# Kernel tuning notes

Measured on AMD Instinct MI355X. Metric: run time of the kernel, lower is better.

Reference implementation:

```python
import jax, jax.numpy as jnp
import numpy as np

B, S, DIM, HEADS, DH = 1, 192, 512, 8, 64
LN_EPS = 1e-5


def setup_inputs() -> dict:
    key = jax.random.key(0)
    ks = jax.random.split(key, 5)
    rn = lambda k, shp: jax.random.normal(k, shp, dtype=jnp.float32) * 0.02
    return {
        "x": jax.random.normal(ks[0], (B, S, DIM), dtype=jnp.float32),
        "ln_w": jnp.ones((DIM,), jnp.float32),
        "ln_b": jnp.zeros((DIM,), jnp.float32),
        "W_abcde": rn(ks[1], (5 * HEADS * DH, DIM)),
        "b_abcde": jnp.zeros((5 * HEADS * DH,), jnp.float32),
        "W_K": rn(ks[2], (HEADS, DH, DH, DH)),
        "W_V": rn(ks[3], (HEADS, DH, DH, DH)),
        "W_out": rn(ks[4], (DIM, HEADS * DH)),
        "b_out": jnp.zeros((DIM,), jnp.float32),
    }


def reference(x, ln_w, ln_b, W_abcde, b_abcde, W_K, W_V, W_out, b_out):
    b, n, _ = x.shape
    # LayerNorm (biased variance, eps=1e-5, affine)
    mu = jnp.mean(x, axis=-1, keepdims=True)
    var = jnp.var(x, axis=-1, keepdims=True)
    xn = (x - mu) / jnp.sqrt(var + LN_EPS) * ln_w + ln_b
    # abcde projection, chunk into 5, split heads -> [b, n, h, d]
    proj = xn @ W_abcde.T + b_abcde
    a_, b_, c_, d_, e_ = [t.reshape(b, n, HEADS, DH) for t in jnp.split(proj, 5, axis=-1)]
    # cubic attention score chain (note: heads summed out in step2, reintroduced by a_)
    step1 = jnp.einsum('brnk,nijk->brij', c_, W_K)          # [b, r, d, d]
    step2 = jnp.einsum('brij,bqnj->briq', step1, b_)        # [b, r, d, q] (sum over heads of b_)
    attn = jnp.einsum('briq,bpni->bnpqr', step2, a_)        # [b, h, p, q, r]
    # "causal" mask: positions where p >= q set to 1e-6 (faithful to masked_fill_)
    t_idx = jnp.arange(n)[:, None, None]
    s_idx = jnp.arange(n)[None, :, None]
    mask = (t_idx >= s_idx)[None, None]                      # [1,1,p,q,1]
    attn = jnp.where(mask, jnp.float32(1e-6), attn)
    # 'b n p1 p2 p3 -> b n p3 (p1 p2)', scale by 1/dim_head, softmax over (p1 p2)
    attn = attn.transpose(0, 1, 4, 2, 3).reshape(b, HEADS, n, n * n) / DH
    attn = jax.nn.softmax(attn, axis=-1)
    # pairwise values: [b, p1, p2, h, d] -> 'b p s n h -> b n h (p s)'
    v = jnp.einsum('bpnh,bqng,nhgf->bpqnf', d_, e_, W_V)
    v = v.transpose(0, 3, 4, 1, 2).reshape(b, HEADS, DH, n * n)
    # weighted sum over pair axis, merge heads
    z = jnp.einsum('bnql,bnhl->bqnh', attn, v).reshape(b, n, HEADS * DH)
    return z @ W_out.T + b_out
```

## Files before the change

kernel.cpp:

```cpp
#include <hip/hip_runtime.h>
#include <hip/hip_bf16.h>
#include <cstdint>

#define SEQ 192

typedef float f32x4 __attribute__((ext_vector_type(4)));
typedef float f32x8 __attribute__((ext_vector_type(8)));
typedef __bf16 bf16;
typedef __bf16 bf16x8 __attribute__((ext_vector_type(8)));
typedef __bf16 bf16x4 __attribute__((ext_vector_type(4)));

#define MFMA_BF16(a, b, c) __builtin_amdgcn_mfma_f32_16x16x32_bf16(a, b, c, 0, 0, 0)

__device__ __forceinline__ bf16x8 cvt8(f32x8 v) {
  bf16x8 o;
#pragma unroll
  for (int i = 0; i < 8; i++) o[i] = (bf16)v[i];
  return o;
}

__global__ __launch_bounds__(256) void k1_prep(
    const float* __restrict__ x, const float* __restrict__ ln_w, const float* __restrict__ ln_b,
    const float* __restrict__ WV, bf16* __restrict__ xn_bf, bf16* __restrict__ WVt2) {
  int bid = blockIdx.x, tid = threadIdx.x;
  if (bid < 512) {
    int g = bid & 63, hh = bid >> 6;
    __shared__ float ld[64 * 65];
    int f = tid & 63, r4 = tid >> 6;
#pragma unroll
    for (int it = 0; it < 16; it++) {
      int hp = it * 4 + r4;
      ld[hp * 65 + f] = WV[(((size_t)(hh * 64 + hp) * 64 + g) * 64) + f];
    }
    __syncthreads();
    int hp2 = tid & 63;
#pragma unroll
    for (int it = 0; it < 16; it++) {
      int ff = it * 4 + r4;
      WVt2[(size_t)hh * 262144 + (size_t)(ff * 64 + g) * 64 + hp2] = (bf16)ld[hp2 * 65 + ff];
    }
    return;
  }
  bid -= 512;
  {
    int r = bid;
    const float* xr = x + (size_t)r * 512;
    float v0 = xr[tid], v1 = xr[tid + 256];
    float s = v0 + v1, s2 = v0 * v0 + v1 * v1;
#pragma unroll
    for (int off = 32; off > 0; off >>= 1) {
      s += __shfl_down(s, off);
      s2 += __shfl_down(s2, off);
    }
    __shared__ float redS[4], redS2[4];
    int wave = tid >> 6, lane = tid & 63;
    if (lane == 0) { redS[wave] = s; redS2[wave] = s2; }
    __syncthreads();
    float S = redS[0] + redS[1] + redS[2] + redS[3];
    float S2 = redS2[0] + redS2[1] + redS2[2] + redS2[3];
    float mean = S * (1.0f / 512.0f);
    float var = S2 * (1.0f / 512.0f) - mean * mean;
    float rstd = rsqrtf(var + 1e-5f);
    bf16* xnr = xn_bf + (size_t)r * 512;
    xnr[tid] = (bf16)((v0 - mean) * rstd * ln_w[tid] + ln_b[tid]);
    xnr[tid + 256] = (bf16)((v1 - mean) * rstd * ln_w[tid + 256] + ln_b[tid + 256]);
  }
}

template <int MODE>
__device__ __forceinline__ void gemm_body(const bf16* __restrict__ A, const bf16* __restrict__ Bt,
                                          bf16* __restrict__ C1, int N, int K,
                                          int nb, int mb, int tid) {
  int n0 = nb * 64, m0 = mb * 64;
  int wave = tid >> 6, lane = tid & 63;
  int lq = lane >> 4, l16 = lane & 15;
  const bf16* Ap = A + (size_t)(m0 + wave * 16 + l16) * K;
  f32x4 acc[4];
#pragma unroll
  for (int nt = 0; nt < 4; nt++) acc[nt] = (f32x4){0.f, 0.f, 0.f, 0.f};
  for (int k0 = 0; k0 < K; k0 += 32) {
    bf16x8 af = *(const bf16x8*)(Ap + k0 + lq * 8);
#pragma unroll
    for (int nt = 0; nt < 4; nt++) {
      bf16x8 bv = *(const bf16x8*)(Bt + (size_t)(n0 + nt * 16 + l16) * K + k0 + lq * 8);
      acc[nt] = MFMA_BF16(af, bv, acc[nt]);
    }
  }
  int cm = m0 + wave * 16 + lq * 4;
#pragma unroll
  for (int nt = 0; nt < 4; nt++) {
    int n = n0 + nt * 16 + l16;
    if constexpr (MODE == 1) {
#pragma unroll
      for (int rg = 0; rg < 4; rg++) C1[(size_t)(cm + rg) * N + n] = (bf16)acc[nt][rg];
    } else {
      int r = cm >> 6, i0 = cm & 63;
      bf16x4 pk = {(bf16)acc[nt][0], (bf16)acc[nt][1], (bf16)acc[nt][2], (bf16)acc[nt][3]};
      *(bf16x4*)(C1 + (size_t)r * 12288 + (size_t)n * 64 + i0) = pk;
    }
  }
}

__global__ __launch_bounds__(256) void k2_proj(
    const bf16* __restrict__ xn_bf, const float* __restrict__ Wab,
    const float* __restrict__ b_abcde, float* __restrict__ proj, bf16* __restrict__ a_bf,
    bf16* __restrict__ c_bf, bf16* __restrict__ d_bf) {
  int bid = blockIdx.x, tid = threadIdx.x;
  int nb = bid % 40, mb = bid / 40;
  int n0 = nb * 64, m0 = mb * 64;
  int wave = tid >> 6, lane = tid & 63;
  int lq = lane >> 4, l16 = lane & 15;
  const bf16* Ap = xn_bf + (size_t)(m0 + wave * 16 + l16) * 512;
  f32x4 acc[4];
#pragma unroll
  for (int nt = 0; nt < 4; nt++) acc[nt] = (f32x4){0.f, 0.f, 0.f, 0.f};
  for (int k0 = 0; k0 < 512; k0 += 32) {
    bf16x8 af = *(const bf16x8*)(Ap + k0 + lq * 8);
#pragma unroll
    for (int nt = 0; nt < 4; nt++) {
      f32x8 wv = *(const f32x8*)(Wab + (size_t)(n0 + nt * 16 + l16) * 512 + k0 + lq * 8);
      acc[nt] = MFMA_BF16(af, cvt8(wv), acc[nt]);
    }
  }
  int cm = m0 + wave * 16 + lq * 4;
#pragma unroll
  for (int nt = 0; nt < 4; nt++) {
    int n = n0 + nt * 16 + l16;
    int chunk = n >> 9, hcol = (n >> 6) & 7, i = n & 63;
#pragma unroll
    for (int rg = 0; rg < 4; rg++) {
      int m = cm + rg;
      float v = acc[nt][rg] + b_abcde[n];
      proj[(size_t)m * 2560 + n] = v;
      bf16 bv = (bf16)v;
      if (chunk == 0) a_bf[((size_t)hcol * SEQ + m) * 64 + i] = bv;
      else if (chunk == 2) c_bf[(size_t)m * 512 + (n - 1024)] = bv;
      else if (chunk == 3) d_bf[((size_t)hcol * SEQ + m) * 64 + i] = bv;
    }
  }
}

__global__ __launch_bounds__(256) void k3_mid(
    const bf16* __restrict__ c_bf, const float* __restrict__ WK, bf16* __restrict__ s1bf,
    const bf16* __restrict__ d_bf, const bf16* __restrict__ WVt2, bf16* __restrict__ tTt,
    const float* __restrict__ proj, bf16* __restrict__ eT_bf, float* __restrict__ ecum,
    bf16* __restrict__ bsum_bf) {
  __shared__ float el[64 * 65];
  int bid = blockIdx.x, tid = threadIdx.x;
  if (bid < 192) {
    int nb = bid % 64, mb = bid / 64;
    int n0 = nb * 64, m0 = mb * 64;
    int wave = tid >> 6, lane = tid & 63;
    int lq = lane >> 4, l16 = lane & 15;
    const bf16* Ap = c_bf + (size_t)(m0 + wave * 16 + l16) * 512;
    f32x4 acc[4];
#pragma unroll
    for (int nt = 0; nt < 4; nt++) acc[nt] = (f32x4){0.f, 0.f, 0.f, 0.f};
    size_t offn[4];
#pragma unroll
    for (int nt = 0; nt < 4; nt++) {
      int n = n0 + nt * 16 + l16;
      offn[nt] = (size_t)(n >> 6) * 4096 + (size_t)(n & 63) * 64;
    }
    for (int k0 = 0; k0 < 512; k0 += 32) {
      bf16x8 af = *(const bf16x8*)(Ap + k0 + lq * 8);
      size_t kb = (size_t)(k0 >> 6) * 262144 + (k0 & 32) + lq * 8;
#pragma unroll
      for (int nt = 0; nt < 4; nt++) {
        f32x8 wv = *(const f32x8*)(WK + kb + offn[nt]);
        acc[nt] = MFMA_BF16(af, cvt8(wv), acc[nt]);
      }
    }
    int cm = m0 + wave * 16 + lq * 4;
#pragma unroll
    for (int nt = 0; nt < 4; nt++) {
      int n = n0 + nt * 16 + l16;
#pragma unroll
      for (int rg = 0; rg < 4; rg++) s1bf[(size_t)(cm + rg) * 4096 + n] = (bf16)acc[nt][rg];
    }
    return;
  }
  bid -= 192;
  if (bid < 1536) {
    int h = bid / 192, rem = bid % 192;
    gemm_body<1>(d_bf + (size_t)h * 12288, WVt2 + (size_t)h * 262144,
                 tTt + (size_t)h * 786432, 4096, 64, rem % 64, rem / 64, tid);
    return;
  }
  bid -= 1536;
  if (bid < 8) {
    int h = bid;
    float carry = 0.f;
    for (int ch = 0; ch < 3; ch++) {
      int pbase = ch * 64;
      for (int idx = tid; idx < 4096; idx += 256) {
        int pl = idx >> 6, g = idx & 63;
        el[pl * 65 + g] = proj[(size_t)(pbase + pl) * 2560 + 2048 + h * 64 + g];
      }
      __syncthreads();
      for (int idx = tid; idx < 4096; idx += 256) {
        int g = idx >> 6, ql = idx & 63;
        eT_bf[((size_t)h * 64 + g) * SEQ + pbase + ql] = (bf16)el[ql * 65 + g];
      }
      if (tid < 64) {
        float run = carry;
        for (int pl = 0; pl < 64; pl++) {
          run += el[pl * 65 + tid];
          ecum[(size_t)h * 12288 + (pbase + pl) * 64 + tid] = run;
        }
        carry = run;
      }
      __syncthreads();
    }
    return;
  }
  bid -= 8;
  {
    int j = tid & 63, qg = tid >> 6;
#pragma unroll
    for (int qi = 0; qi < 16; qi++) {
      int q = bid * 64 + qg * 16 + qi;
      float s = 0.f;
#pragma unroll
      for (int hh = 0; hh < 8; hh++) s += proj[(size_t)q * 2560 + 512 + hh * 64 + j];
      bsum_bf[q * 64 + j] = (bf16)s;
    }
  }
}

__global__ __launch_bounds__(256) void k4_step2(const bf16* __restrict__ s1bf,
                                                const bf16* __restrict__ bsum_bf,
                                                bf16* __restrict__ s2bf) {
  int bid = blockIdx.x;
  gemm_body<2>(s1bf, bsum_bf, s2bf, 192, 64, bid % 3, bid / 3, threadIdx.x);
}

__global__ __launch_bounds__(256, 3) void k5_attn(
    const bf16* __restrict__ a_bf, const bf16* __restrict__ s2bf,
    const bf16* __restrict__ eT_bf, const float* __restrict__ ecum,
    bf16* __restrict__ ew_bf, float* __restrict__ Lsum) {
  int r = blockIdx.x, h = blockIdx.y;
  int tid = threadIdx.x, wave = tid >> 6, lane = tid & 63;
  int lq = lane >> 4, l16 = lane & 15;
  __shared__ __align__(16) bf16 wch[2][4][3][16 * 40];
  __shared__ float redL[4];
  int pt[3] = {wave, wave + 4, 11 - wave};

  const bf16* ah = a_bf + (size_t)h * 12288;
  const bf16* s2r = s2bf + (size_t)r * 12288;
  const bf16* eh = eT_bf + (size_t)h * 12288;
  const float* ech = ecum + (size_t)h * 12288;

  bf16x8 afr[3][2];
#pragma unroll
  for (int mt = 0; mt < 3; mt++)
#pragma unroll
    for (int kc = 0; kc < 2; kc++)
      afr[mt][kc] = *(const bf16x8*)(ah + (pt[mt] * 16 + l16) * 64 + kc * 32 + lq * 8);

  f32x4 ewacc[3][4];
#pragma unroll
  for (int mt = 0; mt < 3; mt++)
#pragma unroll
    for (int nt = 0; nt < 4; nt++) ewacc[mt][nt] = (f32x4){0.f, 0.f, 0.f, 0.f};
  float lpart = 0.f;

  for (int c = 0; c < 6; c++) {
    if (c * 32 + 31 <= wave * 16) continue;
    int par = c & 1;
    bf16x8 efr[4];
#pragma unroll
    for (int nt = 0; nt < 4; nt++)
      efr[nt] = *(const bf16x8*)(eh + (nt * 16 + l16) * SEQ + c * 32 + lq * 8);
    bf16x8 bq[2][2];
#pragma unroll
    for (int sub = 0; sub < 2; sub++) {
      int q = c * 32 + sub * 16 + l16;
      bq[sub][0] = *(const bf16x8*)(s2r + q * 64 + lq * 8);
      bq[sub][1] = *(const bf16x8*)(s2r + q * 64 + 32 + lq * 8);
    }
    f32x4 sacc[3][2];
#pragma unroll
    for (int mt = 0; mt < 3; mt++) {
      if (c * 32 + 31 <= pt[mt] * 16) continue;
#pragma unroll
      for (int sub = 0; sub < 2; sub++) {
        if (c * 32 + sub * 16 + 15 <= pt[mt] * 16) continue;
        f32x4 sv = (f32x4){0.f, 0.f, 0.f, 0.f};
        sv = MFMA_BF16(afr[mt][0], bq[sub][0], sv);
        sacc[mt][sub] = MFMA_BF16(afr[mt][1], bq[sub][1], sv);
      }
    }
#pragma unroll
    for (int mt = 0; mt < 3; mt++) {
      if (c * 32 + 31 <= pt[mt] * 16) continue;
      bf16* mybuf = &wch[par][wave][mt][0];
#pragma unroll
      for (int sub = 0; sub < 2; sub++) {
        if (c * 32 + sub * 16 + 15 <= pt[mt] * 16) {
#pragma unroll
          for (int rg = 0; rg < 4; rg++) mybuf[(lq * 4 + rg) * 40 + sub * 16 + l16] = (bf16)0.f;
          continue;
        }
        int q = c * 32 + sub * 16 + l16;
        int p0 = pt[mt] * 16 + lq * 4;
#pragma unroll
        for (int rg = 0; rg < 4; rg++) {
          float wv = (q > p0 + rg) ? __expf(sacc[mt][sub][rg] * 0.015625f) : 0.f;
          lpart += wv;
          mybuf[(lq * 4 + rg) * 40 + sub * 16 + l16] = (bf16)wv;
        }
      }
    }
#pragma unroll
    for (int mt = 0; mt < 3; mt++) {
      if (c * 32 + 31 <= pt[mt] * 16) continue;
      bf16x8 wf = *(const bf16x8*)(&wch[par][wave][mt][l16 * 40 + lq * 8]);
#pragma unroll
      for (int nt = 0; nt < 4; nt++) ewacc[mt][nt] = MFMA_BF16(wf, efr[nt], ewacc[mt][nt]);
    }
  }

  bf16* ewout = ew_bf + ((size_t)h * SEQ + r) * 12288;
#pragma unroll
  for (int mt = 0; mt < 3; mt++)
#pragma unroll
    for (int nt = 0; nt < 4; nt++)
#pragma unroll
      for (int rg = 0; rg < 4; rg++) {
        int p = pt[mt] * 16 + lq * 4 + rg;
        int g = nt * 16 + l16;
        ewout[p * 64 + g] = (bf16)(ewacc[mt][nt][rg] + ech[p * 64 + g]);
      }

#pragma unroll
  for (int off = 32; off > 0; off >>= 1) lpart += __shfl_down(lpart, off);
  if (lane == 0) redL[wave] = lpart;
  __syncthreads();
  if (tid == 0) Lsum[h * SEQ + r] = redL[0] + redL[1] + redL[2] + redL[3];
}

__global__ __launch_bounds__(512) void k5b_z(
    const bf16* __restrict__ ew_bf, const bf16* __restrict__ tTt, float* __restrict__ Zpart) {
  int h = blockIdx.x, mt = blockIdx.y, ks = blockIdx.z;
  int tid = threadIdx.x, wave = tid >> 6, lane = tid & 63;
  int lq = lane >> 4, l16 = lane & 15;
  __shared__ float zred[8][16][66];
  const bf16* ewh = ew_bf + ((size_t)h * SEQ + mt * 32) * 12288;
  const bf16* th = tTt + (size_t)h * 786432;
  f32x4 acc[2][4];
#pragma unroll
  for (int m2 = 0; m2 < 2; m2++)
#pragma unroll
    for (int nt = 0; nt < 4; nt++) acc[m2][nt] = (f32x4){0.f, 0.f, 0.f, 0.f};
  for (int jj = 0; jj < 6; jj++) {
    int kc = ks * 48 + wave * 6 + jj;
    int p = kc >> 1, g0 = (kc & 1) * 32;
    bf16x8 af0 = *(const bf16x8*)(ewh + (size_t)l16 * 12288 + kc * 32 + lq * 8);
    bf16x8 af1 = *(const bf16x8*)(ewh + (size_t)(16 + l16) * 12288 + kc * 32 + lq * 8);
#pragma unroll
    for (int nt = 0; nt < 4; nt++) {
      bf16x8 tf = *(const bf16x8*)(th + (size_t)p * 4096 + (nt * 16 + l16) * 64 + g0 + lq * 8);
      acc[0][nt] = MFMA_BF16(af0, tf, acc[0][nt]);
      acc[1][nt] = MFMA_BF16(af1, tf, acc[1][nt]);
    }
  }
#pragma unroll
  for (int m2 = 0; m2 < 2; m2++) {
    if (m2) __syncthreads();
#pragma unroll
    for (int nt = 0; nt < 4; nt++)
#pragma unroll
      for (int rg = 0; rg < 4; rg++) zred[wave][lq * 4 + rg][nt * 16 + l16] = acc[m2][nt][rg];
    __syncthreads();
#pragma unroll
    for (int o = 0; o < 2; o++) {
      int idx = o * 512 + tid;
      int rloc = idx >> 6, f = idx & 63;
      float s = 0.f;
#pragma unroll
      for (int wv = 0; wv < 8; wv++) s += zred[wv][rloc][f];
      Zpart[(size_t)ks * 98304 + (size_t)(mt * 32 + m2 * 16 + rloc) * 512 + h * 64 + f] = s;
    }
  }
}

__global__ __launch_bounds__(256) void k6_out(
    const float* __restrict__ Zpart, const float* __restrict__ Lsum,
    const float* __restrict__ Wout, const float* __restrict__ b_out, float* __restrict__ out) {
  int bid = blockIdx.x, tid = threadIdx.x;
  int nb = bid & 7, mb = bid >> 3;
  int n0 = nb * 64, m0 = mb * 64;
  int wave = tid >> 6, lane = tid & 63;
  int lq = lane >> 4, l16 = lane & 15;
  int m = m0 + wave * 16 + l16;
  f32x4 acc[4];
#pragma unroll
  for (int nt = 0; nt < 4; nt++) acc[nt] = (f32x4){0.f, 0.f, 0.f, 0.f};
  for (int k0 = 0; k0 < 512; k0 += 32) {
    int h = k0 >> 6;
    float L = Lsum[h * SEQ + m] + 18528.0f;
    float rL = 1.0f / L;
    size_t zo = (size_t)m * 512 + k0 + lq * 8;
    f32x8 s = *(const f32x8*)(Zpart + zo);
#pragma unroll
    for (int ks = 1; ks < 8; ks++) s += *(const f32x8*)(Zpart + (size_t)ks * 98304 + zo);
    bf16x8 af = cvt8(s * rL);
#pragma unroll
    for (int nt = 0; nt < 4; nt++) {
      f32x8 wv = *(const f32x8*)(Wout + (size_t)(n0 + nt * 16 + l16) * 512 + k0 + lq * 8);
      acc[nt] = MFMA_BF16(af, cvt8(wv), acc[nt]);
    }
  }
  int cm = m0 + wave * 16 + lq * 4;
#pragma unroll
  for (int nt = 0; nt < 4; nt++) {
    int n = n0 + nt * 16 + l16;
    float bv = b_out[n];
#pragma unroll
    for (int rg = 0; rg < 4; rg++) out[(size_t)(cm + rg) * 512 + n] = acc[nt][rg] + bv;
  }
}

static const size_t OFF_PROJ = 0;
static const size_t OFF_ECUM = 491520;
static const size_t OFF_XN = 589824;
static const size_t OFF_ZPART = 638976;
static const size_t OFF_LSUM = 1425408;
static const size_t OFF_WVT = 2473984;
static const size_t OFF_A = 3522560;
static const size_t OFF_C = 3571712;
static const size_t OFF_D = 3620864;
static const size_t OFF_ET = 3670016;
static const size_t OFF_BSUM = 3719168;
static const size_t OFF_S1 = 3725312;
static const size_t OFF_S2 = 4118528;
static const size_t OFF_TT = 5298176;
static const size_t OFF_EW = 8493056;

extern "C" void kernel_launch(void* const* d_in, const int* in_sizes, int n_in,
                              void* d_out, int out_size, void* d_ws, size_t ws_size,
                              hipStream_t stream) {
  (void)in_sizes; (void)n_in; (void)out_size; (void)ws_size;
  const float* x = (const float*)d_in[0];
  const float* ln_w = (const float*)d_in[1];
  const float* ln_b = (const float*)d_in[2];
  const float* W_abcde = (const float*)d_in[3];
  const float* b_abcde = (const float*)d_in[4];
  const float* W_K = (const float*)d_in[5];
  const float* W_V = (const float*)d_in[6];
  const float* W_out = (const float*)d_in[7];
  const float* b_out = (const float*)d_in[8];
  float* out = (float*)d_out;
  float* ws = (float*)d_ws;

  float* proj = ws + OFF_PROJ;
  float* ecum = ws + OFF_ECUM;
  bf16* xn_bf = (bf16*)(ws + OFF_XN);
  float* Zpart = ws + OFF_ZPART;
  float* Lsum = ws + OFF_LSUM;
  bf16* WVt2 = (bf16*)(ws + OFF_WVT);
  bf16* a_bf = (bf16*)(ws + OFF_A);
  bf16* c_bf = (bf16*)(ws + OFF_C);
  bf16* d_bf = (bf16*)(ws + OFF_D);
  bf16* eT_bf = (bf16*)(ws + OFF_ET);
  bf16* bsum_bf = (bf16*)(ws + OFF_BSUM);
  bf16* s1bf = (bf16*)(ws + OFF_S1);
  bf16* s2bf = (bf16*)(ws + OFF_S2);
  bf16* tTt = (bf16*)(ws + OFF_TT);
  bf16* ew_bf = (bf16*)(ws + OFF_EW);

  k1_prep<<<704, 256, 0, stream>>>(x, ln_w, ln_b, W_V, xn_bf, WVt2);
  k2_proj<<<120, 256, 0, stream>>>(xn_bf, W_abcde, b_abcde, proj, a_bf, c_bf, d_bf);
  k3_mid<<<1739, 256, 0, stream>>>(c_bf, W_K, s1bf, d_bf, WVt2, tTt, proj, eT_bf, ecum,
                                   bsum_bf);
  k4_step2<<<576, 256, 0, stream>>>(s1bf, bsum_bf, s2bf);
  k5_attn<<<dim3(SEQ, 8), 256, 0, stream>>>(a_bf, s2bf, eT_bf, ecum, ew_bf, Lsum);
  k5b_z<<<dim3(8, 6, 8), 512, 0, stream>>>(ew_bf, tTt, Zpart);
  k6_out<<<24, 256, 0, stream>>>(Zpart, Lsum, W_out, b_out, out);
}
```

Baseline: 255.8 us.

## Split Zpart reduction into separate kernel and split-K the output projection

Adds a kernel that sums the eight Zpart partials and normalizes by Lsum, writing a bf16 z matrix. The output projection then reads z directly and splits the K dimension across four waves, reducing their results through shared memory. Its grid grows from 24 to 96 blocks. This spreads the out-projection over more CUs and stops it redundantly re-reducing the partials for every n-block, at the cost of one extra kernel launch and an extra global round-trip for z.

After: 214.9 us. -16.0%, faster.

```diff
diff --git a/kernel.cpp b/kernel.cpp
--- a/kernel.cpp
+++ b/kernel.cpp
@@ -385,40 +385,55 @@
   }
 }
 
+__global__ __launch_bounds__(256) void k5c_zf(const float* __restrict__ Zpart,
+                                              const float* __restrict__ Lsum,
+                                              bf16* __restrict__ z_bf) {
+  int m = blockIdx.x, tid = threadIdx.x;
+#pragma unroll
+  for (int o = 0; o < 2; o++) {
+    int c = o * 256 + tid;
+    int h = c >> 6;
+    float s = 0.f;
+#pragma unroll
+    for (int ks = 0; ks < 8; ks++) s += Zpart[(size_t)ks * 98304 + (size_t)m * 512 + c];
+    float L = Lsum[h * SEQ + m] + 18528.0f;
+    z_bf[(size_t)m * 512 + c] = (bf16)(s / L);
+  }
+}
+
 __global__ __launch_bounds__(256) void k6_out(
-    const float* __restrict__ Zpart, const float* __restrict__ Lsum,
-    const float* __restrict__ Wout, const float* __restrict__ b_out, float* __restrict__ out) {
+    const bf16* __restrict__ z_bf, const float* __restrict__ Wout,
+    const float* __restrict__ b_out, float* __restrict__ out) {
   int bid = blockIdx.x, tid = threadIdx.x;
   int nb = bid & 7, mb = bid >> 3;
-  int n0 = nb * 64, m0 = mb * 64;
   int wave = tid >> 6, lane = tid & 63;
   int lq = lane >> 4, l16 = lane & 15;
-  int m = m0 + wave * 16 + l16;
+  int m = mb * 16 + l16;
   f32x4 acc[4];
 #pragma unroll
   for (int nt = 0; nt < 4; nt++) acc[nt] = (f32x4){0.f, 0.f, 0.f, 0.f};
-  for (int k0 = 0; k0 < 512; k0 += 32) {
-    int h = k0 >> 6;
-    float L = Lsum[h * SEQ + m] + 18528.0f;
-    float rL = 1.0f / L;
-    size_t zo = (size_t)m * 512 + k0 + lq * 8;
-    f32x8 s = *(const f32x8*)(Zpart + zo);
-#pragma unroll
-    for (int ks = 1; ks < 8; ks++) s += *(const f32x8*)(Zpart + (size_t)ks * 98304 + zo);
-    bf16x8 af = cvt8(s * rL);
-#pragma unroll
-    for (int nt = 0; nt < 4; nt++) {
-      f32x8 wv = *(const f32x8*)(Wout + (size_t)(n0 + nt * 16 + l16) * 512 + k0 + lq * 8);
+#pragma unroll
+  for (int kc = 0; kc < 4; kc++) {
+    int k0 = wave * 128 + kc * 32;
+    bf16x8 af = *(const bf16x8*)(z_bf + (size_t)m * 512 + k0 + lq * 8);
+#pragma unroll
+    for (int nt = 0; nt < 4; nt++) {
+      f32x8 wv = *(const f32x8*)(Wout + (size_t)(nb * 64 + nt * 16 + l16) * 512 + k0 + lq * 8);
       acc[nt] = MFMA_BF16(af, cvt8(wv), acc[nt]);
     }
   }
-  int cm = m0 + wave * 16 + lq * 4;
-#pragma unroll
-  for (int nt = 0; nt < 4; nt++) {
-    int n = n0 + nt * 16 + l16;
-    float bv = b_out[n];
-#pragma unroll
-    for (int rg = 0; rg < 4; rg++) out[(size_t)(cm + rg) * 512 + n] = acc[nt][rg] + bv;
+  __shared__ float red[4][16][68];
+#pragma unroll
+  for (int nt = 0; nt < 4; nt++)
+#pragma unroll
+    for (int rg = 0; rg < 4; rg++) red[wave][lq * 4 + rg][nt * 16 + l16] = acc[nt][rg];
+  __syncthreads();
+#pragma unroll
+  for (int o = 0; o < 4; o++) {
+    int idx = o * 256 + tid;
+    int rloc = idx >> 6, f = idx & 63;
+    float s = red[0][rloc][f] + red[1][rloc][f] + red[2][rloc][f] + red[3][rloc][f];
+    out[(size_t)(mb * 16 + rloc) * 512 + nb * 64 + f] = s + b_out[nb * 64 + f];
   }
 }
 
@@ -427,6 +442,7 @@
 static const size_t OFF_XN = 589824;
 static const size_t OFF_ZPART = 638976;
 static const size_t OFF_LSUM = 1425408;
+static const size_t OFF_Z = 1427456;
 static const size_t OFF_WVT = 2473984;
 static const size_t OFF_A = 3522560;
 static const size_t OFF_C = 3571712;
@@ -459,6 +475,7 @@
   bf16* xn_bf = (bf16*)(ws + OFF_XN);
   float* Zpart = ws + OFF_ZPART;
   float* Lsum = ws + OFF_LSUM;
+  bf16* z_bf = (bf16*)(ws + OFF_Z);
   bf16* WVt2 = (bf16*)(ws + OFF_WVT);
   bf16* a_bf = (bf16*)(ws + OFF_A);
   bf16* c_bf = (bf16*)(ws + OFF_C);
@@ -477,5 +494,6 @@
   k4_step2<<<576, 256, 0, stream>>>(s1bf, bsum_bf, s2bf);
   k5_attn<<<dim3(SEQ, 8), 256, 0, stream>>>(a_bf, s2bf, eT_bf, ecum, ew_bf, Lsum);
   k5b_z<<<dim3(8, 6, 8), 512, 0, stream>>>(ew_bf, tTt, Zpart);
-  k6_out<<<24, 256, 0, stream>>>(Zpart, Lsum, W_out, b_out, out);
-}
+  k5c_zf<<<SEQ, 256, 0, stream>>>(Zpart, Lsum, z_bf);
+  k6_out<<<96, 256, 0, stream>>>(z_bf, W_out, b_out, out);
+}
```
